# Kernel tuning notes

Measured on AMD Instinct MI355X. Metric: run time of the kernel, lower is better.

The kernel has to match this reference:

```python
import jax, jax.numpy as jnp
import numpy as np

MASS, CHARGE, ALPHA, BETA = 1.0, 0.5, 0.1, 0.05
ETA = jnp.array([1.0, -1.0, -1.0, -1.0], dtype=jnp.float32)  # Minkowski metric diag


def setup_inputs() -> dict:
    key = jax.random.key(0)
    k1, k2, k3 = jax.random.split(key, 3)
    B = 262144
    y = jax.random.normal(k1, (B, 8), dtype=jnp.float32)
    W = jax.random.normal(k2, (4, 4), dtype=jnp.float32) * 0.3
    V = jax.random.normal(k3, (4, 4), dtype=jnp.float32) * 0.3
    return {"y": y, "W": W, "V": V}


def _lagrangian(z):
    # z = (x, u, A) concatenated, shape [12]
    x, u, A = z[0:4], z[4:8], z[8:12]
    kinetic = 0.5 * MASS * jnp.sum(ETA * u * u)
    coupling = CHARGE * jnp.sum(ETA * u * A)
    xu_term = ALPHA * jnp.sum((x * u) ** 2)      # makes J_xu nontrivial
    uA_term = BETA * jnp.sum(u * A) ** 2          # makes J_Au nontrivial
    return kinetic + coupling + xu_term + uA_term


def reference(y, W, V):
    def A_vec(x):  # vector potential A^mu(x), works on [4] or [B,4]
        return jnp.tanh(x @ W.T) + x @ V.T

    x = y[:, 0:4]   # [B,4] positions
    u = y[:, 4:8]   # [B,4] velocities
    A = A_vec(x)    # [B,4]
    z = jnp.concatenate([x, u, A], axis=1)  # [B,12] = (x,u,A)

    gradL = jax.vmap(jax.grad(_lagrangian))(z)      # [B,12]
    H = jax.vmap(jax.hessian(_lagrangian))(z)       # [B,12,12]

    dL_dx = gradL[:, 0:4]
    dL_dA = gradL[:, 8:12]
    J_xu = H[:, 0:4, 4:8]    # d^2L/(dx^mu du^nu)
    J_uu = H[:, 4:8, 4:8]    # d^2L/(du^mu du^nu)
    J_Au = H[:, 8:12, 4:8]   # d^2L/(dA^mu du^nu)

    # dA_dx[a, nu, i] = dA^i/dx^nu (matches tf.stack(..., axis=2) layout)
    jacA = jax.vmap(jax.jacfwd(A_vec))(x)           # [B, i, nu]
    dA_dx = jnp.transpose(jacA, (0, 2, 1))          # [B, nu, i]

    J_uu_inv = jnp.linalg.pinv(J_uu)                # [B,4,4]

    force = (dL_dx
             + jnp.einsum('ajk,ak->aj', dA_dx, dL_dA)
             - jnp.einsum('ai,aij->aj', u,
                          J_xu + jnp.einsum('ajk,akm->ajm', dA_dx, J_Au)))
    acceleration = jnp.einsum('ai,aij->aj', force, J_uu_inv)  # [B,4]
    return acceleration
```

## Files before the change

kernel.cpp:

```cpp
#include <hip/hip_runtime.h>
#include <math.h>


#define SIX_RCOND 2.86102294921875e-5
#define RCOND     4.76837158203125e-6
#define MAXSLOW   8

__device__ __forceinline__ void model_terms(
    const double* sW, const double* sV,
    const double x[4], const double u[4],
    double A[4], double f[4], double d[4])
{
    const double eta[4] = {1.0, -1.0, -1.0, -1.0};
    const double CHG = 0.5, ALPHA = 0.1, BETA = 0.05;
    double G[4][4];
    #pragma unroll
    for (int j = 0; j < 4; ++j) {
        double t = 0.0, s = 0.0;
        #pragma unroll
        for (int k = 0; k < 4; ++k) { t += sW[j*4+k]*x[k]; s += sV[j*4+k]*x[k]; }
        double th = tanh(t);
        A[j] = th + s;
        double dth = 1.0 - th * th;
        #pragma unroll
        for (int k = 0; k < 4; ++k) G[j][k] = dth * sW[j*4+k] + sV[j*4+k];
    }
    double S = 0.0;
    #pragma unroll
    for (int k = 0; k < 4; ++k) S += u[k] * A[k];
    double P[4], R[4], Q[4];
    #pragma unroll
    for (int j = 0; j < 4; ++j) {
        double p = 0.0, r = 0.0, q = 0.0;
        #pragma unroll
        for (int k = 0; k < 4; ++k) {
            p += G[k][j] * u[k];
            r += G[j][k] * u[k];
            q += G[k][j] * (CHG * eta[k]) * u[k];
        }
        P[j] = p; R[j] = r; Q[j] = q;
    }
    double T = 0.0;
    #pragma unroll
    for (int j = 0; j < 4; ++j) T += u[j] * R[j];
    #pragma unroll
    for (int j = 0; j < 4; ++j) {
        f[j] = -2.0 * ALPHA * x[j] * u[j] * u[j]
             + Q[j]
             + 2.0 * BETA * S * P[j]
             - (CHG * eta[j] + 2.0 * BETA * S) * R[j]
             - 2.0 * BETA * A[j] * T;
        d[j] = eta[j] + 2.0 * ALPHA * x[j] * x[j];
    }
}

__device__ __forceinline__ void sm_solve(
    const double d[4], const double A[4], const double f[4], double acc[4])
{
    const double C2 = 0.1;
    double b[4], fd[4], den = 1.0, w = 0.0;
    #pragma unroll
    for (int j = 0; j < 4; ++j) {
        double inv = 1.0 / d[j];
        b[j]  = A[j] * inv;
        fd[j] = f[j] * inv;
        den  += C2 * A[j] * b[j];
        w    += b[j] * f[j];
    }
    double scale = C2 * w / den;
    #pragma unroll
    for (int j = 0; j < 4; ++j) acc[j] = fd[j] - b[j] * scale;
}

__device__ void jacobi_pinv_solve(
    const double d[4], const double A[4], const double f[4], double acc[4])
{
    const double C2 = 0.1;
    double M[4][4], Vm[4][4];
    #pragma unroll
    for (int r = 0; r < 4; ++r) {
        #pragma unroll
        for (int c = 0; c < 4; ++c) {
            M[r][c] = C2 * A[r] * A[c];
            Vm[r][c] = (r == c) ? 1.0 : 0.0;
        }
        M[r][r] += d[r];
    }
    for (int sweep = 0; sweep < 5; ++sweep) {
        #pragma unroll
        for (int p = 0; p < 3; ++p) {
            #pragma unroll
            for (int q2 = p + 1; q2 < 4; ++q2) {
                double apq = M[p][q2];
                if (fabs(apq) < 1e-280) continue;
                double app = M[p][p], aqq = M[q2][q2];
                double tau = (aqq - app) / (2.0 * apq);
                double tt = ((tau >= 0.0) ? 1.0 : -1.0) /
                            (fabs(tau) + sqrt(1.0 + tau * tau));
                double c = 1.0 / sqrt(1.0 + tt * tt);
                double s = tt * c;
                #pragma unroll
                for (int k = 0; k < 4; ++k) {
                    double mkp = M[k][p], mkq = M[k][q2];
                    M[k][p]  = c * mkp - s * mkq;
                    M[k][q2] = s * mkp + c * mkq;
                }
                #pragma unroll
                for (int k = 0; k < 4; ++k) {
                    double mpk = M[p][k], mqk = M[q2][k];
                    M[p][k]  = c * mpk - s * mqk;
                    M[q2][k] = s * mpk + c * mqk;
                }
                #pragma unroll
                for (int k = 0; k < 4; ++k) {
                    double vkp = Vm[k][p], vkq = Vm[k][q2];
                    Vm[k][p]  = c * vkp - s * vkq;
                    Vm[k][q2] = s * vkp + c * vkq;
                }
            }
        }
    }
    double lam[4], sigmax = 0.0;
    #pragma unroll
    for (int k = 0; k < 4; ++k) {
        lam[k] = M[k][k];
        double a = fabs(lam[k]);
        sigmax = (a > sigmax) ? a : sigmax;
    }
    double cutoff = RCOND * sigmax;
    #pragma unroll
    for (int j = 0; j < 4; ++j) acc[j] = 0.0;
    #pragma unroll
    for (int e = 0; e < 4; ++e) {
        if (fabs(lam[e]) > cutoff) {
            double coef = 0.0;
            #pragma unroll
            for (int k = 0; k < 4; ++k) coef += Vm[k][e] * f[k];
            coef /= lam[e];
            #pragma unroll
            for (int j = 0; j < 4; ++j) acc[j] += coef * Vm[j][e];
        }
    }
}

__global__ __launch_bounds__(256) void rel_particle_kernel(
    const float* __restrict__ y, const float* __restrict__ W,
    const float* __restrict__ V, float* __restrict__ out, int B)
{
    __shared__ double sW[16], sV[16];
    __shared__ double stash[MAXSLOW][12];
    __shared__ int    sidx[MAXSLOW];
    __shared__ int    scnt;

    int tid = threadIdx.x;
    if (tid < 16)      sW[tid]      = (double)W[tid];
    else if (tid < 32) sV[tid - 16] = (double)V[tid - 16];
    if (tid == 32) scnt = 0;
    __syncthreads();

    int i = blockIdx.x * blockDim.x + tid;
    if (i < B) {
        const float4* y4 = (const float4*)y;
        float4 xv = y4[2 * i];
        float4 uv = y4[2 * i + 1];
        double x[4] = {xv.x, xv.y, xv.z, xv.w};
        double u[4] = {uv.x, uv.y, uv.z, uv.w};

        double A[4], f[4], d[4];
        model_terms(sW, sV, x, u, A, f, d);

        const double C2 = 0.1;
        double mind = 1e300;
        #pragma unroll
        for (int j = 0; j < 4; ++j) {
            double a = fabs(d[j]);
            mind = (a < mind) ? a : mind;
        }
        double p01 = d[0] * d[1], p23 = d[2] * d[3];
        double det = p01 * p23
            + C2 * (A[0]*A[0]*(d[1]*p23) + A[1]*A[1]*(d[0]*p23) +
                    A[2]*A[2]*(p01*d[3]) + A[3]*A[3]*(p01*d[2]));
        double sumA2 = 0.0, sumA4 = 0.0, F2 = 0.0;
        #pragma unroll
        for (int j = 0; j < 4; ++j) {
            double Aj2 = A[j] * A[j];
            sumA2 += Aj2; sumA4 += Aj2 * Aj2;
            double Jjj = d[j] + C2 * Aj2;
            F2 += Jjj * Jjj;
        }
        F2 += C2 * C2 * (sumA2 * sumA2 - sumA4);
        double rowmax = 0.0;
        #pragma unroll
        for (int r = 0; r < 4; ++r) {
            double rs = 0.0;
            #pragma unroll
            for (int c = 0; c < 4; ++c) {
                double Jrc = C2 * A[r] * A[c] + ((r == c) ? d[r] : 0.0);
                rs += fabs(Jrc);
            }
            rowmax = (rs > rowmax) ? rs : rowmax;
        }
        double sig_hi2 = rowmax * rowmax;
        sig_hi2 = (F2 < sig_hi2) ? F2 : sig_hi2;
        bool safe = (fabs(det) > SIX_RCOND * sig_hi2 * sig_hi2) && (mind > 1e-3);

        if (safe) {
            double acc[4];
            sm_solve(d, A, f, acc);
            float4 res;
            res.x = (float)acc[0]; res.y = (float)acc[1];
            res.z = (float)acc[2]; res.w = (float)acc[3];
            ((float4*)out)[i] = res;
        } else {
            int k = atomicAdd(&scnt, 1);
            if (k < MAXSLOW) {
                sidx[k] = i;
                #pragma unroll
                for (int j = 0; j < 4; ++j) {
                    stash[k][j]     = A[j];
                    stash[k][4 + j] = f[j];
                    stash[k][8 + j] = d[j];
                }
            } else {
                double acc[4];
                sm_solve(d, A, f, acc);
                float4 res;
                res.x = (float)acc[0]; res.y = (float)acc[1];
                res.z = (float)acc[2]; res.w = (float)acc[3];
                ((float4*)out)[i] = res;
            }
        }
    }
    __syncthreads();

    int n = scnt;
    if (n > MAXSLOW) n = MAXSLOW;
    if (tid < n) {
        double A[4], f[4], d[4];
        #pragma unroll
        for (int j = 0; j < 4; ++j) {
            A[j] = stash[tid][j];
            f[j] = stash[tid][4 + j];
            d[j] = stash[tid][8 + j];
        }
        double acc[4];
        jacobi_pinv_solve(d, A, f, acc);
        float4 res;
        res.x = (float)acc[0]; res.y = (float)acc[1];
        res.z = (float)acc[2]; res.w = (float)acc[3];
        ((float4*)out)[sidx[tid]] = res;
    }
}

extern "C" void kernel_launch(void* const* d_in, const int* in_sizes, int n_in,
                              void* d_out, int out_size, void* d_ws, size_t ws_size,
                              hipStream_t stream) {
    const float* y = (const float*)d_in[0];
    const float* W = (const float*)d_in[1];
    const float* V = (const float*)d_in[2];
    float* out = (float*)d_out;
    int B = in_sizes[0] / 8;
    int block = 256;
    int grid = (B + block - 1) / block;
    rel_particle_kernel<<<grid, block, 0, stream>>>(y, W, V, out, B);
}
```

Measured before the change: 88.61 us.

## Run fast path in fp32 and recompute rare slow cases in fp64

The common path now computes the model terms, conditioning test and Sherman-Morrison solve in fp32 instead of fp64, with a retuned determinant safety threshold. Flagged ill-conditioned elements no longer stash fp64 intermediates in shared memory. Instead they reload their inputs and recompute everything in fp64 before the Jacobi pseudo-inverse. The overflow path now uses the full fp64 pinv rather than the fast solve, and the slot count grows from 8 to 16. This trades fp64 throughput for fp32 and risks accuracy near the threshold, since the fp32 conditioning test may misclassify borderline cases.

```diff
diff --git a/kernel.cpp b/kernel.cpp
--- a/kernel.cpp
+++ b/kernel.cpp
@@ -2,11 +2,11 @@
 #include <math.h>
 
 
-#define SIX_RCOND 2.86102294921875e-5
-#define RCOND     4.76837158203125e-6
-#define MAXSLOW   8
-
-__device__ __forceinline__ void model_terms(
+#define RCOND        4.76837158203125e-6
+#define SAFE_DET_F32 8.0e-5f
+#define MAXSLOW      16
+
+__device__ void model_terms_f64(
     const double* sW, const double* sV,
     const double x[4], const double u[4],
     double A[4], double f[4], double d[4])
@@ -52,24 +52,6 @@
              - 2.0 * BETA * A[j] * T;
         d[j] = eta[j] + 2.0 * ALPHA * x[j] * x[j];
     }
-}
-
-__device__ __forceinline__ void sm_solve(
-    const double d[4], const double A[4], const double f[4], double acc[4])
-{
-    const double C2 = 0.1;
-    double b[4], fd[4], den = 1.0, w = 0.0;
-    #pragma unroll
-    for (int j = 0; j < 4; ++j) {
-        double inv = 1.0 / d[j];
-        b[j]  = A[j] * inv;
-        fd[j] = f[j] * inv;
-        den  += C2 * A[j] * b[j];
-        w    += b[j] * f[j];
-    }
-    double scale = C2 * w / den;
-    #pragma unroll
-    for (int j = 0; j < 4; ++j) acc[j] = fd[j] - b[j] * scale;
 }
 
 __device__ void jacobi_pinv_solve(
@@ -147,83 +129,135 @@
     const float* __restrict__ y, const float* __restrict__ W,
     const float* __restrict__ V, float* __restrict__ out, int B)
 {
-    __shared__ double sW[16], sV[16];
-    __shared__ double stash[MAXSLOW][12];
+    __shared__ float  sWf[16], sVf[16];
+    __shared__ double sWd[16], sVd[16];
     __shared__ int    sidx[MAXSLOW];
     __shared__ int    scnt;
 
     int tid = threadIdx.x;
-    if (tid < 16)      sW[tid]      = (double)W[tid];
-    else if (tid < 32) sV[tid - 16] = (double)V[tid - 16];
+    if (tid < 16) {
+        float w = W[tid];
+        sWf[tid] = w; sWd[tid] = (double)w;
+    } else if (tid < 32) {
+        float v = V[tid - 16];
+        sVf[tid - 16] = v; sVd[tid - 16] = (double)v;
+    }
     if (tid == 32) scnt = 0;
     __syncthreads();
 
     int i = blockIdx.x * blockDim.x + tid;
+    float4 xv, uv;
     if (i < B) {
         const float4* y4 = (const float4*)y;
-        float4 xv = y4[2 * i];
-        float4 uv = y4[2 * i + 1];
-        double x[4] = {xv.x, xv.y, xv.z, xv.w};
-        double u[4] = {uv.x, uv.y, uv.z, uv.w};
-
-        double A[4], f[4], d[4];
-        model_terms(sW, sV, x, u, A, f, d);
-
-        const double C2 = 0.1;
-        double mind = 1e300;
+        xv = y4[2 * i];
+        uv = y4[2 * i + 1];
+        float x[4] = {xv.x, xv.y, xv.z, xv.w};
+        float u[4] = {uv.x, uv.y, uv.z, uv.w};
+        const float eta[4] = {1.f, -1.f, -1.f, -1.f};
+        const float CHG = 0.5f, ALPHA = 0.1f, BETA = 0.05f, C2 = 0.1f;
+
+        float A[4], G[4][4];
         #pragma unroll
         for (int j = 0; j < 4; ++j) {
-            double a = fabs(d[j]);
+            float t = 0.f, s = 0.f;
+            #pragma unroll
+            for (int k = 0; k < 4; ++k) {
+                t += sWf[j*4+k] * x[k];
+                s += sVf[j*4+k] * x[k];
+            }
+            float th = tanhf(t);
+            A[j] = th + s;
+            float dth = 1.f - th * th;
+            #pragma unroll
+            for (int k = 0; k < 4; ++k) G[j][k] = dth * sWf[j*4+k] + sVf[j*4+k];
+        }
+        float S = 0.f;
+        #pragma unroll
+        for (int k = 0; k < 4; ++k) S += u[k] * A[k];
+        float P[4], R[4], Q[4];
+        #pragma unroll
+        for (int j = 0; j < 4; ++j) {
+            float p = 0.f, r = 0.f, q = 0.f;
+            #pragma unroll
+            for (int k = 0; k < 4; ++k) {
+                p += G[k][j] * u[k];
+                r += G[j][k] * u[k];
+                q += G[k][j] * (CHG * eta[k]) * u[k];
+            }
+            P[j] = p; R[j] = r; Q[j] = q;
+        }
+        float T = 0.f;
+        #pragma unroll
+        for (int j = 0; j < 4; ++j) T += u[j] * R[j];
+        float f[4], d[4];
+        float mind = 1e30f;
+        #pragma unroll
+        for (int j = 0; j < 4; ++j) {
+            f[j] = -2.f * ALPHA * x[j] * u[j] * u[j]
+                 + Q[j]
+                 + 2.f * BETA * S * P[j]
+                 - (CHG * eta[j] + 2.f * BETA * S) * R[j]
+                 - 2.f * BETA * A[j] * T;
+            d[j] = eta[j] + 2.f * ALPHA * x[j] * x[j];
+            float a = fabsf(d[j]);
             mind = (a < mind) ? a : mind;
         }
-        double p01 = d[0] * d[1], p23 = d[2] * d[3];
-        double det = p01 * p23
+
+        float p01 = d[0]*d[1], p23 = d[2]*d[3];
+        float det = p01 * p23
             + C2 * (A[0]*A[0]*(d[1]*p23) + A[1]*A[1]*(d[0]*p23) +
                     A[2]*A[2]*(p01*d[3]) + A[3]*A[3]*(p01*d[2]));
-        double sumA2 = 0.0, sumA4 = 0.0, F2 = 0.0;
+        float sumA2 = 0.f, sumA4 = 0.f, F2 = 0.f;
         #pragma unroll
         for (int j = 0; j < 4; ++j) {
-            double Aj2 = A[j] * A[j];
-            sumA2 += Aj2; sumA4 += Aj2 * Aj2;
-            double Jjj = d[j] + C2 * Aj2;
-            F2 += Jjj * Jjj;
-        }
-        F2 += C2 * C2 * (sumA2 * sumA2 - sumA4);
-        double rowmax = 0.0;
+            float Aj2 = A[j]*A[j];
+            sumA2 += Aj2; sumA4 += Aj2*Aj2;
+            float Jjj = d[j] + C2*Aj2;
+            F2 += Jjj*Jjj;
+        }
+        F2 += C2*C2*(sumA2*sumA2 - sumA4);
+        float rowmax = 0.f;
         #pragma unroll
         for (int r = 0; r < 4; ++r) {
-            double rs = 0.0;
+            float rs = 0.f;
             #pragma unroll
             for (int c = 0; c < 4; ++c) {
-                double Jrc = C2 * A[r] * A[c] + ((r == c) ? d[r] : 0.0);
-                rs += fabs(Jrc);
+                float Jrc = C2*A[r]*A[c] + ((r == c) ? d[r] : 0.f);
+                rs += fabsf(Jrc);
             }
             rowmax = (rs > rowmax) ? rs : rowmax;
         }
-        double sig_hi2 = rowmax * rowmax;
-        sig_hi2 = (F2 < sig_hi2) ? F2 : sig_hi2;
-        bool safe = (fabs(det) > SIX_RCOND * sig_hi2 * sig_hi2) && (mind > 1e-3);
+        float sig2 = rowmax*rowmax;
+        sig2 = (F2 < sig2) ? F2 : sig2;
+        bool safe = (fabsf(det) > SAFE_DET_F32 * sig2 * sig2) && (mind > 1e-3f);
 
         if (safe) {
-            double acc[4];
-            sm_solve(d, A, f, acc);
+            float b[4], fd[4], den = 1.f, w = 0.f;
+            #pragma unroll
+            for (int j = 0; j < 4; ++j) {
+                float inv = 1.f / d[j];
+                b[j]  = A[j] * inv;
+                fd[j] = f[j] * inv;
+                den  += C2 * A[j] * b[j];
+                w    += b[j] * f[j];
+            }
+            float scale = C2 * w / den;
             float4 res;
-            res.x = (float)acc[0]; res.y = (float)acc[1];
-            res.z = (float)acc[2]; res.w = (float)acc[3];
+            res.x = fd[0] - b[0]*scale;
+            res.y = fd[1] - b[1]*scale;
+            res.z = fd[2] - b[2]*scale;
+            res.w = fd[3] - b[3]*scale;
             ((float4*)out)[i] = res;
         } else {
             int k = atomicAdd(&scnt, 1);
             if (k < MAXSLOW) {
                 sidx[k] = i;
-                #pragma unroll
-                for (int j = 0; j < 4; ++j) {
-                    stash[k][j]     = A[j];
-                    stash[k][4 + j] = f[j];
-                    stash[k][8 + j] = d[j];
-                }
             } else {
-                double acc[4];
-                sm_solve(d, A, f, acc);
+                double xd[4] = {xv.x, xv.y, xv.z, xv.w};
+                double ud[4] = {uv.x, uv.y, uv.z, uv.w};
+                double Ad[4], fdd[4], dd[4], acc[4];
+                model_terms_f64(sWd, sVd, xd, ud, Ad, fdd, dd);
+                jacobi_pinv_solve(dd, Ad, fdd, acc);
                 float4 res;
                 res.x = (float)acc[0]; res.y = (float)acc[1];
                 res.z = (float)acc[2]; res.w = (float)acc[3];
@@ -236,19 +270,19 @@
     int n = scnt;
     if (n > MAXSLOW) n = MAXSLOW;
     if (tid < n) {
-        double A[4], f[4], d[4];
-        #pragma unroll
-        for (int j = 0; j < 4; ++j) {
-            A[j] = stash[tid][j];
-            f[j] = stash[tid][4 + j];
-            d[j] = stash[tid][8 + j];
-        }
-        double acc[4];
-        jacobi_pinv_solve(d, A, f, acc);
+        int pi = sidx[tid];
+        const float4* y4 = (const float4*)y;
+        float4 xw = y4[2 * pi];
+        float4 uw = y4[2 * pi + 1];
+        double xd[4] = {xw.x, xw.y, xw.z, xw.w};
+        double ud[4] = {uw.x, uw.y, uw.z, uw.w};
+        double Ad[4], fdd[4], dd[4], acc[4];
+        model_terms_f64(sWd, sVd, xd, ud, Ad, fdd, dd);
+        jacobi_pinv_solve(dd, Ad, fdd, acc);
         float4 res;
         res.x = (float)acc[0]; res.y = (float)acc[1];
         res.z = (float)acc[2]; res.w = (float)acc[3];
-        ((float4*)out)[sidx[tid]] = res;
+        ((float4*)out)[pi] = res;
     }
 }
 
```

Measured after the change: 88.56 us. About the same (-0.1%).
